# Performance work log

Measured on AMD Instinct MI355X. Metric: run time of the kernel, lower is better.

The kernel has to match this reference:

```python
import jax, jax.numpy as jnp
import numpy as np

D = 1024      # hidden_size
H = 16        # num_attention_heads
HD = D // H   # head_dim
FF = 4096     # intermediate_size
EPS = 1e-5

def layernorm(x, g, b):
    mu = jnp.mean(x, axis=-1, keepdims=True)
    var = jnp.mean(jnp.square(x - mu), axis=-1, keepdims=True)
    return (x - mu) * jax.lax.rsqrt(var + EPS) * g + b

def setup_inputs() -> dict:
    key = jax.random.key(0)
    ks = jax.random.split(key, 16)
    s = 0.02
    return {
        "x":   jax.random.normal(ks[0], (4, 1024, D), jnp.float32),
        "wq":  jax.random.normal(ks[1], (D, D), jnp.float32) * s,
        "bq":  jnp.zeros((D,), jnp.float32),
        "wk":  jax.random.normal(ks[2], (D, D), jnp.float32) * s,
        "bk":  jnp.zeros((D,), jnp.float32),
        "wv":  jax.random.normal(ks[3], (D, D), jnp.float32) * s,
        "bv":  jnp.zeros((D,), jnp.float32),
        "wo":  jax.random.normal(ks[4], (D, D), jnp.float32) * s,
        "bo":  jnp.zeros((D,), jnp.float32),
        "w1":  jax.random.normal(ks[5], (D, FF), jnp.float32) * s,
        "b1":  jnp.zeros((FF,), jnp.float32),
        "w2":  jax.random.normal(ks[6], (FF, D), jnp.float32) * s,
        "b2":  jnp.zeros((D,), jnp.float32),
        "ln1_g": jnp.ones((D,), jnp.float32),
        "ln1_b": jnp.zeros((D,), jnp.float32),
        "ln2_g": jnp.ones((D,), jnp.float32),
        "ln2_b": jnp.zeros((D,), jnp.float32),
    }

def reference(x, wq, bq, wk, bk, wv, bv, wo, bo, w1, b1, w2, b2,
              ln1_g, ln1_b, ln2_g, ln2_b):
    B, S, _ = x.shape
    # --- pre-LN multi-head attention (per-head linears fused as one GEMM) ---
    h = layernorm(x, ln1_g, ln1_b)
    q = (h @ wq + bq).reshape(B, S, H, HD).transpose(0, 2, 1, 3)  # [B,H,S,hd]
    k = (h @ wk + bk).reshape(B, S, H, HD).transpose(0, 2, 1, 3)
    v = (h @ wv + bv).reshape(B, S, H, HD).transpose(0, 2, 1, 3)
    scores = jnp.einsum('bhqd,bhkd->bhqk', q, k) / np.sqrt(HD).astype(x.dtype)
    weights = jax.nn.softmax(scores, axis=-1)  # dropout p=0 -> identity
    attn = jnp.einsum('bhqk,bhkd->bhqd', weights, v)
    attn = attn.transpose(0, 2, 1, 3).reshape(B, S, D)
    x = x + attn @ wo + bo
    # --- pre-LN feed-forward with exact GELU ---
    h2 = layernorm(x, ln2_g, ln2_b)
    ffn = jax.nn.gelu(h2 @ w1 + b1, approximate=False) @ w2 + b2
    return x + ffn
```

## Files before the change

### kernel.cpp

```cpp
#include <hip/hip_runtime.h>
#include <hip/hip_bf16.h>
#include <cstdint>

#define S_LEN  1024
#define DMODEL 1024
#define NTOK   4096
#define NHEAD  16
#define HDIM   64
#define FFDIM  4096
#define NBATCH 4

using bf16x8 = __attribute__((ext_vector_type(8))) short;
using f32x4  = __attribute__((ext_vector_type(4))) float;

__device__ __forceinline__ ushort f2bf(float f) {
  union { float f; uint32_t u; } a; a.f = f;
  uint32_t u = a.u;
  u += 0x7FFFu + ((u >> 16) & 1u);
  return (ushort)(u >> 16);
}
__device__ __forceinline__ float bf2f(ushort u) {
  union { uint32_t u; float f; } c; c.u = ((uint32_t)u) << 16; return c.f;
}
__device__ __forceinline__ float ld_as_float(const float* p, long i) { return p[i]; }
__device__ __forceinline__ float ld_as_float(const ushort* p, long i) { return bf2f(p[i]); }
__device__ __forceinline__ void st_out(float* C, long i, float v) { C[i] = v; }
__device__ __forceinline__ void st_out(ushort* C, long i, float v) { C[i] = f2bf(v); }

__device__ __forceinline__ void gld_lds16(const void* g, void* l) {
  __builtin_amdgcn_global_load_lds((const __attribute__((address_space(1))) void*)g,
                                   (__attribute__((address_space(3))) void*)l, 16, 0, 0);
}

__global__ __launch_bounds__(256) void ln_kernel(const float* __restrict__ x,
    const float* __restrict__ g, const float* __restrict__ b,
    ushort* __restrict__ out) {
  int row = blockIdx.x;
  int tid = threadIdx.x;
  const float4* xr = (const float4*)(x + (long)row * DMODEL);
  float4 v = xr[tid];
  float s  = v.x + v.y + v.z + v.w;
  float s2 = v.x*v.x + v.y*v.y + v.z*v.z + v.w*v.w;
  for (int off = 32; off; off >>= 1) { s += __shfl_down(s, off); s2 += __shfl_down(s2, off); }
  __shared__ float red[8];
  int wid = tid >> 6, lane = tid & 63;
  if (lane == 0) { red[wid] = s; red[wid + 4] = s2; }
  __syncthreads();
  if (tid == 0) {
    red[0] = red[0] + red[1] + red[2] + red[3];
    red[4] = red[4] + red[5] + red[6] + red[7];
  }
  __syncthreads();
  float mu  = red[0] * (1.0f / DMODEL);
  float var = red[4] * (1.0f / DMODEL) - mu * mu;
  float rs  = rsqrtf(var + 1e-5f);
  float4 gg = ((const float4*)g)[tid];
  float4 bb = ((const float4*)b)[tid];
  ushort4 o;
  o.x = f2bf((v.x - mu) * rs * gg.x + bb.x);
  o.y = f2bf((v.y - mu) * rs * gg.y + bb.y);
  o.z = f2bf((v.z - mu) * rs * gg.z + bb.z);
  o.w = f2bf((v.w - mu) * rs * gg.w + bb.w);
  ((ushort4*)(out + (long)row * DMODEL))[tid] = o;
}

__global__ __launch_bounds__(256) void concat3(const float* __restrict__ a,
    const float* __restrict__ b, const float* __restrict__ c, float* __restrict__ o) {
  int i = blockIdx.x * 256 + threadIdx.x;
  o[i] = (i < 1024) ? a[i] : ((i < 2048) ? b[i - 1024] : c[i - 2048]);
}

template <int NP, bool XRES>
__global__ __launch_bounds__(256) void reduce_add(
    const ushort* __restrict__ parts, const float* __restrict__ xres,
    const float* __restrict__ bias, float* __restrict__ out) {
  long i = (long)blockIdx.x * 256 + threadIdx.x;
  const long PSTRIDE = (long)NTOK * DMODEL / 4;
  float4 acc = XRES ? ((const float4*)xres)[i] : ((const float4*)out)[i];
  float4 b = ((const float4*)bias)[i & 255];
  acc.x += b.x; acc.y += b.y; acc.z += b.z; acc.w += b.w;
#pragma unroll
  for (int z = 0; z < NP; ++z) {
    ushort4 u = ((const ushort4*)parts)[z * PSTRIDE + i];
    acc.x += bf2f(u.x); acc.y += bf2f(u.y); acc.z += bf2f(u.z); acc.w += bf2f(u.w);
  }
  ((float4*)out)[i] = acc;
}

template <typename TIN>
__global__ __launch_bounds__(256) void transpose_cvt(const TIN* __restrict__ in,
    ushort* __restrict__ out, int ldin, int ldout,
    long inZhi, long inZlo, long outZ) {
  int z = blockIdx.z;
  in  += (long)(z >> 4) * inZhi + (long)(z & 15) * inZlo;
  out += (long)z * outZ;
  __shared__ float tile[32][33];
  int c0 = blockIdx.x * 32, r0 = blockIdx.y * 32;
  int tx = threadIdx.x, ty = threadIdx.y;
  for (int i = ty; i < 32; i += 8)
    tile[i][tx] = ld_as_float(in, (long)(r0 + i) * ldin + c0 + tx);
  __syncthreads();
  for (int i = ty; i < 32; i += 8)
    out[(long)(c0 + i) * ldout + r0 + tx] = f2bf(tile[tx][i]);
}

template <int ACT, bool BIAS, bool RES, typename TOUT>
__global__ __launch_bounds__(256) void gemm_bt(
    const ushort* __restrict__ A, const ushort* __restrict__ BT, TOUT* __restrict__ C,
    const float* __restrict__ bias, const float* __restrict__ resp,
    int M, int K, int lda, int ldb, int ldc,
    long aZhi, long aZlo, long bZhi, long bZlo, long cZhi, long cZlo) {
  __shared__ __align__(16) ushort lA[2][128 * 64];
  __shared__ __align__(16) ushort lB[2][128 * 64];
  int z = blockIdx.z;
  A  += (long)(z >> 4) * aZhi + (long)(z & 15) * aZlo;
  BT += (long)(z >> 4) * bZhi + (long)(z & 15) * bZlo;
  long coff = (long)(z >> 4) * cZhi + (long)(z & 15) * cZlo;
  int gx = gridDim.x;
  int nwg = gx * gridDim.y;
  int lin = blockIdx.x + gx * blockIdx.y;
  int wg = (lin & 7) * (nwg >> 3) + (lin >> 3);
  int n0 = (wg / gx) * 128, m0 = (wg % gx) * 128;
  int tid = threadIdx.x, lane = tid & 63, wid = tid >> 6;
  int wr = wid >> 1, wc = wid & 1;
  int lrow = lane >> 3;
  int swz = ((lane & 7) ^ lrow) << 3;
  int Mm1 = M - 1;
  f32x4 acc[4][4];
#pragma unroll
  for (int i = 0; i < 4; i++)
#pragma unroll
    for (int j = 0; j < 4; j++) acc[i][j] = (f32x4){0.f, 0.f, 0.f, 0.f};

  auto STAGE = [&](int kt, int buf) {
    const ushort* Ak = A + (kt << 6) + swz;
    const ushort* Bk = BT + (kt << 6) + swz;
#pragma unroll
    for (int c = 0; c < 4; ++c) {
      int ch = (wid << 2) | c;
      int rb = (ch << 3) + lrow;
      gld_lds16(Ak + (long)(n0 + rb) * lda, &lA[buf][ch << 9]);
      int mrow = min(m0 + rb, Mm1);
      gld_lds16(Bk + (long)mrow * ldb, &lB[buf][ch << 9]);
    }
  };

  int nK = K >> 6;
  STAGE(0, 0);
  for (int kt = 0; kt < nK; ++kt) {
    int cur = kt & 1;
    if (kt + 1 < nK) {
      STAGE(kt + 1, cur ^ 1);
      asm volatile("s_waitcnt vmcnt(8)" ::: "memory");
    } else {
      asm volatile("s_waitcnt vmcnt(0)" ::: "memory");
    }
    __builtin_amdgcn_s_barrier();
    __builtin_amdgcn_sched_barrier(0);
#pragma unroll
    for (int kk = 0; kk < 2; ++kk) {
      int g = (kk << 2) | (lane >> 4);
      int kfs = ((g ^ (lane & 7)) << 3);
      bf16x8 af[4], bfr[4];
#pragma unroll
      for (int i = 0; i < 4; i++) {
        af[i]  = *(const bf16x8*)(&lA[cur][((wr << 6) + (i << 4) + (lane & 15)) * 64 + kfs]);
        bfr[i] = *(const bf16x8*)(&lB[cur][((wc << 6) + (i << 4) + (lane & 15)) * 64 + kfs]);
      }
#pragma unroll
      for (int i = 0; i < 4; i++)
#pragma unroll
        for (int j = 0; j < 4; j++)
          acc[i][j] = __builtin_amdgcn_mfma_f32_16x16x32_bf16(af[i], bfr[j], acc[i][j], 0, 0, 0);
    }
    asm volatile("s_waitcnt lgkmcnt(0)" ::: "memory");
    __builtin_amdgcn_s_barrier();
    __builtin_amdgcn_sched_barrier(0);
  }
#pragma unroll
  for (int i = 0; i < 4; i++) {
    int rbase = n0 + wr * 64 + i * 16 + ((lane >> 4) << 2);
#pragma unroll
    for (int j = 0; j < 4; j++) {
      int col = m0 + wc * 64 + j * 16 + (lane & 15);
      if (col < M) {
        float bv = BIAS ? bias[col] : 0.0f;
#pragma unroll
        for (int q = 0; q < 4; q++) {
          int rowg = rbase + q;
          float vv = acc[i][j][q] + bv;
          if (ACT == 1) vv = 0.5f * vv * (1.0f + erff(vv * 0.70710678118f));
          long idx = coff + (long)rowg * ldc + col;
          if (RES) vv += resp[idx];
          st_out(C, idx, vv);
        }
      }
    }
  }
}

template <int ACT, bool BIAS, typename TOUT>
__global__ __launch_bounds__(512, 2) void gemm256(
    const ushort* __restrict__ A, const ushort* __restrict__ BT, TOUT* __restrict__ C,
    const float* __restrict__ bias,
    int K, int lda, int ldb, int ldc, long aZlo, long bZlo, long cZlo) {
  __shared__ __align__(16) ushort lA[2][256 * 64];
  __shared__ __align__(16) ushort lB[2][256 * 64];
  int z = blockIdx.z;
  A  += (long)z * aZlo;
  BT += (long)z * bZlo;
  C  += (long)z * cZlo;
  int gx = gridDim.x;
  int nwg = gx * gridDim.y;
  int lin = blockIdx.x + gx * blockIdx.y;
  int wg = (lin & 7) * (nwg >> 3) + (lin >> 3);
  int n0 = (wg / gx) * 256, m0 = (wg % gx) * 256;
  int tid = threadIdx.x, lane = tid & 63, wid = tid >> 6;
  int wm = wid >> 2, wn = wid & 3;
  int lo = lane & 15, hi = lane >> 4;
  int l7 = lane & 7;
  int srow = tid >> 3;
  int skg  = (tid & 7) ^ (srow & 7);
  const ushort* gA = A + (long)(n0 + srow) * lda + (skg << 3);
  const ushort* gB = BT + (long)(m0 + srow) * ldb + (skg << 3);

  f32x4 acc[8][4];
#pragma unroll
  for (int i = 0; i < 8; ++i)
#pragma unroll
    for (int j = 0; j < 4; ++j) acc[i][j] = (f32x4){0.f, 0.f, 0.f, 0.f};

  auto STG = [&](int kt, int buf, int c) {
    if (c < 4)
      gld_lds16(gA + (long)(c * 64) * lda + (kt << 6), &lA[buf][c * 4096 + wid * 512]);
    else
      gld_lds16(gB + (long)((c - 4) * 64) * ldb + (kt << 6), &lB[buf][(c - 4) * 4096 + wid * 512]);
  };

  int nK = K >> 6;
  STG(0, 0, 4); STG(0, 0, 5); STG(0, 0, 6); STG(0, 0, 7);
  STG(0, 0, 0); STG(0, 0, 1); STG(0, 0, 2); STG(0, 0, 3);
  STG(1, 1, 4); STG(1, 1, 5); STG(1, 1, 6); STG(1, 1, 7);
  asm volatile("s_waitcnt vmcnt(4)" ::: "memory");
  __builtin_amdgcn_s_barrier();

  for (int t = 0; t < nK; ++t) {
    int cur = t & 1, nxt = cur ^ 1;
    ushort* plA = &lA[cur][0];
    ushort* plB = &lB[cur][0];
    bf16x8 bfr[4][2];
#pragma unroll
    for (int p = 0; p < 4; ++p) {
      if (p == 0) {
#pragma unroll
        for (int j = 0; j < 4; ++j)
#pragma unroll
          for (int kk = 0; kk < 2; ++kk)
            bfr[j][kk] = *(const bf16x8*)&plB[(wn * 64 + j * 16 + lo) * 64 +
                                             ((((kk << 2) | hi) ^ l7) << 3)];
      }
      bf16x8 afr[2][2];
#pragma unroll
      for (int ii = 0; ii < 2; ++ii)
#pragma unroll
        for (int kk = 0; kk < 2; ++kk)
          afr[ii][kk] = *(const bf16x8*)&plA[(wm * 128 + (p * 2 + ii) * 16 + lo) * 64 +
                                             ((((kk << 2) | hi) ^ l7) << 3)];
      if (p == 0 && t + 1 < nK) { STG(t + 1, nxt, 0); STG(t + 1, nxt, 1); }
      if (p == 1 && t + 1 < nK) { STG(t + 1, nxt, 2); STG(t + 1, nxt, 3); }
      if (p == 2 && t + 2 < nK) { STG(t + 2, cur, 4); STG(t + 2, cur, 5); }
      if (p == 3 && t + 2 < nK) { STG(t + 2, cur, 6); STG(t + 2, cur, 7); }
      __builtin_amdgcn_s_barrier();
      asm volatile("s_waitcnt lgkmcnt(0)" ::: "memory");
      __builtin_amdgcn_sched_barrier(0);
      __builtin_amdgcn_s_setprio(1);
#pragma unroll
      for (int ii = 0; ii < 2; ++ii)
#pragma unroll
        for (int j = 0; j < 4; ++j)
#pragma unroll
          for (int kk = 0; kk < 2; ++kk)
            acc[p * 2 + ii][j] = __builtin_amdgcn_mfma_f32_16x16x32_bf16(
                afr[ii][kk], bfr[j][kk], acc[p * 2 + ii][j], 0, 0, 0);
      __builtin_amdgcn_s_setprio(0);
      __builtin_amdgcn_sched_barrier(0);
      if (p == 3 && t + 1 < nK) {
        if (t + 2 < nK) asm volatile("s_waitcnt vmcnt(4)" ::: "memory");
        else            asm volatile("s_waitcnt vmcnt(0)" ::: "memory");
      }
      __builtin_amdgcn_s_barrier();
    }
  }

#pragma unroll
  for (int i = 0; i < 8; ++i) {
    int rbase = n0 + wm * 128 + i * 16 + hi * 4;
#pragma unroll
    for (int j = 0; j < 4; ++j) {
      int colg = m0 + wn * 64 + j * 16 + lo;
      float bv = BIAS ? bias[colg] : 0.0f;
#pragma unroll
      for (int q = 0; q < 4; ++q) {
        float vv = acc[i][j][q] + bv;
        if (ACT == 1) vv = 0.5f * vv * (1.0f + erff(vv * 0.70710678118f));
        long idx = (long)(rbase + q) * ldc + colg;
        st_out(C, idx, vv);
      }
    }
  }
}

#define QBLK 64
#define KBLK 128
__global__ __launch_bounds__(256) void flash_attn(
    const ushort* __restrict__ qkv, const ushort* __restrict__ vt,
    ushort* __restrict__ attn) {
  __shared__ __align__(16) ushort lK[2][KBLK * 64];
  __shared__ __align__(16) ushort lV[2][64 * KBLK];
  __shared__ __align__(16) ushort lP[4 * 16 * KBLK];

  int qt = blockIdx.x, bh = blockIdx.z;
  int b = bh >> 4, hh = bh & 15;
  int tid = threadIdx.x, lane = tid & 63, wid = tid >> 6;
  int lo = lane & 15, hi = lane >> 4;
  int lrow = lane >> 3;
  int swz8 = ((lane & 7) ^ lrow) << 3;

  const ushort* Qg = qkv + (long)(b * 1024 + qt * QBLK) * 3072 + hh * 64;
  const ushort* Kg = qkv + (long)(b * 1024) * 3072 + 1024 + hh * 64;
  const ushort* Vg = vt + (long)bh * 64 * 1024;
  ushort* lPw = lP + wid * (16 * KBLK);

  auto STAGE = [&](int t, int buf) {
#pragma unroll
    for (int c = 0; c < 4; ++c) {
      int ch = (wid << 2) | c;
      int rb = (ch << 3) + lrow;
      gld_lds16(Kg + (long)(t * KBLK + rb) * 3072 + swz8, &lK[buf][ch << 9]);
    }
#pragma unroll
    for (int c = 0; c < 4; ++c) {
      int ch = (wid << 2) | c;
      int hd = (ch << 2) + hi;
      gld_lds16(Vg + (long)hd * 1024 + t * KBLK + ((lo ^ (hd & 7)) << 3), &lV[buf][ch << 9]);
    }
  };

#pragma unroll
  for (int c = 0; c < 2; ++c) {
    int ch = wid * 2 + c;
    int rb = ch * 8 + lrow;
    gld_lds16(Qg + (long)rb * 3072 + swz8, &lP[ch << 9]);
  }
  STAGE(0, 0);
  asm volatile("s_waitcnt vmcnt(8)" ::: "memory");
  __builtin_amdgcn_sched_barrier(0);
  bf16x8 a_q[2];
#pragma unroll
  for (int kk = 0; kk < 2; ++kk)
    a_q[kk] = *(const bf16x8*)&lP[(wid * 16 + lo) * 64 + (((kk * 4 + hi) ^ (lo & 7)) << 3)];
  asm volatile("s_waitcnt lgkmcnt(0)" ::: "memory");
  __builtin_amdgcn_sched_barrier(0);
  __builtin_amdgcn_s_barrier();

  float m_run[4], l_run[4];
#pragma unroll
  for (int q = 0; q < 4; ++q) { m_run[q] = -1e30f; l_run[q] = 0.0f; }
  f32x4 acc_o[4];
#pragma unroll
  for (int j = 0; j < 4; ++j) acc_o[j] = (f32x4){0.f, 0.f, 0.f, 0.f};

  for (int t = 0; t < 8; ++t) {
    int cur = t & 1;
    if (t + 1 < 8) {
      STAGE(t + 1, cur ^ 1);
      asm volatile("s_waitcnt vmcnt(8)" ::: "memory");
    } else {
      asm volatile("s_waitcnt vmcnt(0)" ::: "memory");
    }
    __builtin_amdgcn_s_barrier();
    __builtin_amdgcn_sched_barrier(0);

    f32x4 s[8];
#pragma unroll
    for (int j = 0; j < 8; ++j) s[j] = (f32x4){0.f, 0.f, 0.f, 0.f};
#pragma unroll
    for (int kk = 0; kk < 2; ++kk) {
      int slot = ((kk * 4 + hi) ^ (lo & 7)) << 3;
#pragma unroll
      for (int j = 0; j < 8; ++j) {
        bf16x8 bk = *(const bf16x8*)&lK[cur][(j * 16 + lo) * 64 + slot];
        s[j] = __builtin_amdgcn_mfma_f32_16x16x32_bf16(a_q[kk], bk, s[j], 0, 0, 0);
      }
    }
#pragma unroll
    for (int j = 0; j < 8; ++j)
#pragma unroll
      for (int q = 0; q < 4; ++q) s[j][q] *= 0.125f;

    float alpha[4];
#pragma unroll
    for (int q = 0; q < 4; ++q) {
      float m = fmaxf(fmaxf(fmaxf(s[0][q], s[1][q]), fmaxf(s[2][q], s[3][q])),
                      fmaxf(fmaxf(s[4][q], s[5][q]), fmaxf(s[6][q], s[7][q])));
#pragma unroll
      for (int off = 1; off < 16; off <<= 1) m = fmaxf(m, __shfl_xor(m, off));
      float mnew = fmaxf(m_run[q], m);
      alpha[q] = __expf(m_run[q] - mnew);
      m_run[q] = mnew;
    }
    float psum[4] = {0.f, 0.f, 0.f, 0.f};
#pragma unroll
    for (int j = 0; j < 8; ++j)
#pragma unroll
      for (int q = 0; q < 4; ++q) {
        float e = __expf(s[j][q] - m_run[q]);
        psum[q] += e;
        int row = hi * 4 + q;
        int col = j * 16 + lo;
        lPw[row * KBLK + (col ^ ((row & 7) << 3))] = f2bf(e);
      }
#pragma unroll
    for (int q = 0; q < 4; ++q) {
#pragma unroll
      for (int off = 1; off < 16; off <<= 1) psum[q] += __shfl_xor(psum[q], off);
      l_run[q] = l_run[q] * alpha[q] + psum[q];
    }

#pragma unroll
    for (int j = 0; j < 4; ++j)
#pragma unroll
      for (int q = 0; q < 4; ++q) acc_o[j][q] *= alpha[q];
#pragma unroll
    for (int ks = 0; ks < 4; ++ks) {
      int slot = ((ks * 4 + hi) ^ (lo & 7)) << 3;
      bf16x8 ap = *(const bf16x8*)&lPw[lo * KBLK + slot];
#pragma unroll
      for (int j = 0; j < 4; ++j) {
        bf16x8 bv = *(const bf16x8*)&lV[cur][(j * 16 + lo) * KBLK + slot];
        acc_o[j] = __builtin_amdgcn_mfma_f32_16x16x32_bf16(ap, bv, acc_o[j], 0, 0, 0);
      }
    }
    asm volatile("s_waitcnt lgkmcnt(0)" ::: "memory");
    __builtin_amdgcn_s_barrier();
    __builtin_amdgcn_sched_barrier(0);
  }

#pragma unroll
  for (int q = 0; q < 4; ++q) {
    float linv = 1.0f / l_run[q];
    int qrow = qt * QBLK + wid * 16 + hi * 4 + q;
#pragma unroll
    for (int j = 0; j < 4; ++j)
      attn[(long)(b * 1024 + qrow) * 1024 + hh * 64 + j * 16 + lo] = f2bf(acc_o[j][q] * linv);
  }
}

extern "C" void kernel_launch(void* const* d_in, const int* in_sizes, int n_in,
                              void* d_out, int out_size, void* d_ws, size_t ws_size,
                              hipStream_t stream) {
  const float* x    = (const float*)d_in[0];
  const float* wq   = (const float*)d_in[1];
  const float* bq   = (const float*)d_in[2];
  const float* wk   = (const float*)d_in[3];
  const float* bk   = (const float*)d_in[4];
  const float* wv   = (const float*)d_in[5];
  const float* bv   = (const float*)d_in[6];
  const float* wo   = (const float*)d_in[7];
  const float* bo   = (const float*)d_in[8];
  const float* w1   = (const float*)d_in[9];
  const float* b1   = (const float*)d_in[10];
  const float* w2   = (const float*)d_in[11];
  const float* b2   = (const float*)d_in[12];
  const float* ln1g = (const float*)d_in[13];
  const float* ln1b = (const float*)d_in[14];
  const float* ln2g = (const float*)d_in[15];
  const float* ln2b = (const float*)d_in[16];
  float* out = (float*)d_out;

  char* ws = (char*)d_ws;
  size_t off = 0;
  auto alloc = [&](size_t bytes) { void* p = ws + off; off += (bytes + 255) & ~(size_t)255; return p; };
  ushort* h     = (ushort*)alloc((size_t)NTOK * DMODEL * 2);
  ushort* wqkvT = (ushort*)alloc((size_t)3 * DMODEL * DMODEL * 2);
  ushort* woT   = (ushort*)alloc((size_t)DMODEL * DMODEL * 2);
  float*  bqkv  = (float*)alloc((size_t)3 * DMODEL * 4);
  ushort* qkv   = (ushort*)alloc((size_t)NTOK * 3 * DMODEL * 2);
  ushort* vt    = (ushort*)alloc((size_t)64 * HDIM * S_LEN * 2);
  ushort* attn  = (ushort*)alloc((size_t)NTOK * DMODEL * 2);
  ushort* w1T   = (ushort*)alloc((size_t)DMODEL * FFDIM * 2);
  ushort* w2T   = (ushort*)alloc((size_t)FFDIM * DMODEL * 2);
  ushort* gact  = (ushort*)alloc((size_t)NTOK * FFDIM * 2);
  ushort* woPart  = qkv;
  ushort* ffnPart = qkv;

  dim3 tb32(32, 8);
  hipLaunchKernelGGL((transpose_cvt<float>), dim3(DMODEL/32, DMODEL/32, 1), tb32, 0, stream,
                     wq, wqkvT, DMODEL, DMODEL, 0, 0, 0);
  hipLaunchKernelGGL((transpose_cvt<float>), dim3(DMODEL/32, DMODEL/32, 1), tb32, 0, stream,
                     wk, wqkvT + (size_t)DMODEL * DMODEL, DMODEL, DMODEL, 0, 0, 0);
  hipLaunchKernelGGL((transpose_cvt<float>), dim3(DMODEL/32, DMODEL/32, 1), tb32, 0, stream,
                     wv, wqkvT + (size_t)2 * DMODEL * DMODEL, DMODEL, DMODEL, 0, 0, 0);
  hipLaunchKernelGGL((transpose_cvt<float>), dim3(DMODEL/32, DMODEL/32, 1), tb32, 0, stream,
                     wo, woT, DMODEL, DMODEL, 0, 0, 0);
  hipLaunchKernelGGL(concat3, dim3(12), dim3(256), 0, stream, bq, bk, bv, bqkv);

  hipLaunchKernelGGL(ln_kernel, dim3(NTOK), dim3(256), 0, stream, x, ln1g, ln1b, h);

  hipLaunchKernelGGL((gemm256<0, true, ushort>), dim3(12, 16, 1), dim3(512), 0, stream,
                     h, wqkvT, qkv, bqkv, DMODEL, DMODEL, DMODEL, 3 * DMODEL, 0L, 0L, 0L);

  hipLaunchKernelGGL((transpose_cvt<ushort>), dim3(HDIM/32, S_LEN/32, 64), tb32, 0, stream,
                     qkv + 2 * DMODEL, vt, 3 * DMODEL, S_LEN,
                     (long)S_LEN * 3 * DMODEL, 64L, (long)HDIM * S_LEN);

  hipLaunchKernelGGL(flash_attn, dim3(16, 1, 64), dim3(256), 0, stream, qkv, vt, attn);

  hipLaunchKernelGGL((gemm_bt<0, false, false, ushort>), dim3(8, 32, 2), dim3(256), 0, stream,
                     attn, woT, woPart, (const float*)nullptr, (const float*)nullptr,
                     DMODEL, 512, DMODEL, DMODEL, DMODEL,
                     0L, 512L, 0L, 512L, 0L, (long)NTOK * DMODEL);
  hipLaunchKernelGGL((reduce_add<2, true>), dim3(4096), dim3(256), 0, stream,
                     woPart, x, bo, out);
  hipLaunchKernelGGL(ln_kernel, dim3(NTOK), dim3(256), 0, stream, out, ln2g, ln2b, h);
  hipLaunchKernelGGL((transpose_cvt<float>), dim3(FFDIM/32, DMODEL/32, 1), tb32, 0, stream,
                     w1, w1T, FFDIM, DMODEL, 0, 0, 0);
  hipLaunchKernelGGL((transpose_cvt<float>), dim3(DMODEL/32, FFDIM/32, 1), tb32, 0, stream,
                     w2, w2T, DMODEL, FFDIM, 0, 0, 0);
  hipLaunchKernelGGL((gemm256<1, true, ushort>), dim3(16, 16, 1), dim3(512), 0, stream,
                     h, w1T, gact, b1, DMODEL, DMODEL, DMODEL, FFDIM, 0L, 0L, 0L);
  hipLaunchKernelGGL((gemm256<0, false, ushort>), dim3(4, 16, 4), dim3(512), 0, stream,
                     gact, w2T, ffnPart, (const float*)nullptr,
                     1024, FFDIM, FFDIM, DMODEL, 1024L, 1024L, (long)NTOK * DMODEL);
  hipLaunchKernelGGL((reduce_add<4, false>), dim3(4096), dim3(256), 0, stream,
                     ffnPart, (const float*)nullptr, b2, out);
  (void)in_sizes; (void)n_in; (void)out_size; (void)ws_size;
}
```

Measured before the change: 264.8 us.

## Fold softmax scale into Q GEMM, MFMA row sums, fuse residual-reduce with LN2

The QKV GEMM epilogue now multiplies Q columns by log2(e)/sqrt(hd), so flash attention can use exp2 without a per-score scale multiply. The softmax row sum is computed by an extra MFMA against a ones vector instead of shuffle reductions. The kernel also uses a hardware bf16 convert and adds s_setprio hints around the MFMA blocks. Separately, the attention-output reduction and the second layernorm are fused into one kernel, removing one full pass over the activations. In exchange, Q is rounded to bf16 after scaling and the row sum is built from bf16-rounded probabilities.

```diff
diff --git a/kernel.cpp b/kernel.cpp
--- a/kernel.cpp
+++ b/kernel.cpp
@@ -9,6 +9,7 @@
 #define HDIM   64
 #define FFDIM  4096
 #define NBATCH 4
+#define QSCALE 0.1803368801f
 
 using bf16x8 = __attribute__((ext_vector_type(8))) short;
 using f32x4  = __attribute__((ext_vector_type(4))) float;
@@ -18,6 +19,11 @@
   uint32_t u = a.u;
   u += 0x7FFFu + ((u >> 16) & 1u);
   return (ushort)(u >> 16);
+}
+__device__ __forceinline__ ushort f2bf_hw(float f) {
+  uint32_t r;
+  asm("v_cvt_pk_bf16_f32 %0, %1, %1" : "=v"(r) : "v"(f));
+  return (ushort)r;
 }
 __device__ __forceinline__ float bf2f(ushort u) {
   union { uint32_t u; float f; } c; c.u = ((uint32_t)u) << 16; return c.f;
@@ -70,13 +76,13 @@
   o[i] = (i < 1024) ? a[i] : ((i < 2048) ? b[i - 1024] : c[i - 2048]);
 }
 
-template <int NP, bool XRES>
+template <int NP>
 __global__ __launch_bounds__(256) void reduce_add(
-    const ushort* __restrict__ parts, const float* __restrict__ xres,
-    const float* __restrict__ bias, float* __restrict__ out) {
+    const ushort* __restrict__ parts, const float* __restrict__ bias,
+    float* __restrict__ out) {
   long i = (long)blockIdx.x * 256 + threadIdx.x;
   const long PSTRIDE = (long)NTOK * DMODEL / 4;
-  float4 acc = XRES ? ((const float4*)xres)[i] : ((const float4*)out)[i];
+  float4 acc = ((const float4*)out)[i];
   float4 b = ((const float4*)bias)[i & 255];
   acc.x += b.x; acc.y += b.y; acc.z += b.z; acc.w += b.w;
 #pragma unroll
@@ -85,6 +91,49 @@
     acc.x += bf2f(u.x); acc.y += bf2f(u.y); acc.z += bf2f(u.z); acc.w += bf2f(u.w);
   }
   ((float4*)out)[i] = acc;
+}
+
+template <int NP>
+__global__ __launch_bounds__(256) void reduce_ln(
+    const ushort* __restrict__ parts, const float* __restrict__ xres,
+    const float* __restrict__ bias, float* __restrict__ out,
+    const float* __restrict__ g, const float* __restrict__ bln,
+    ushort* __restrict__ hout) {
+  int row = blockIdx.x, tid = threadIdx.x;
+  long i = (long)row * 256 + tid;
+  const long PSTRIDE = (long)NTOK * DMODEL / 4;
+  float4 v = ((const float4*)xres)[i];
+  float4 b = ((const float4*)bias)[tid];
+  v.x += b.x; v.y += b.y; v.z += b.z; v.w += b.w;
+#pragma unroll
+  for (int z = 0; z < NP; ++z) {
+    ushort4 u = ((const ushort4*)parts)[z * PSTRIDE + i];
+    v.x += bf2f(u.x); v.y += bf2f(u.y); v.z += bf2f(u.z); v.w += bf2f(u.w);
+  }
+  ((float4*)out)[i] = v;
+  float s  = v.x + v.y + v.z + v.w;
+  float s2 = v.x*v.x + v.y*v.y + v.z*v.z + v.w*v.w;
+  for (int off = 32; off; off >>= 1) { s += __shfl_down(s, off); s2 += __shfl_down(s2, off); }
+  __shared__ float red[8];
+  int wid = tid >> 6, lane = tid & 63;
+  if (lane == 0) { red[wid] = s; red[wid + 4] = s2; }
+  __syncthreads();
+  if (tid == 0) {
+    red[0] = red[0] + red[1] + red[2] + red[3];
+    red[4] = red[4] + red[5] + red[6] + red[7];
+  }
+  __syncthreads();
+  float mu  = red[0] * (1.0f / DMODEL);
+  float var = red[4] * (1.0f / DMODEL) - mu * mu;
+  float rs  = rsqrtf(var + 1e-5f);
+  float4 gg = ((const float4*)g)[tid];
+  float4 bb = ((const float4*)bln)[tid];
+  ushort4 o;
+  o.x = f2bf((v.x - mu) * rs * gg.x + bb.x);
+  o.y = f2bf((v.y - mu) * rs * gg.y + bb.y);
+  o.z = f2bf((v.z - mu) * rs * gg.z + bb.z);
+  o.w = f2bf((v.w - mu) * rs * gg.w + bb.w);
+  ((ushort4*)hout)[i] = o;
 }
 
 template <typename TIN>
@@ -303,6 +352,7 @@
       for (int q = 0; q < 4; ++q) {
         float vv = acc[i][j][q] + bv;
         if (ACT == 1) vv = 0.5f * vv * (1.0f + erff(vv * 0.70710678118f));
+        if (ACT == 2 && colg < DMODEL) vv *= QSCALE;
         long idx = (long)(rbase + q) * ldc + colg;
         st_out(C, idx, vv);
       }
@@ -331,6 +381,10 @@
   const ushort* Vg = vt + (long)bh * 64 * 1024;
   ushort* lPw = lP + wid * (16 * KBLK);
 
+  bf16x8 kOnes;
+#pragma unroll
+  for (int i = 0; i < 8; ++i) kOnes[i] = (short)0x3F80;
+
   auto STAGE = [&](int t, int buf) {
 #pragma unroll
     for (int c = 0; c < 4; ++c) {
@@ -363,12 +417,13 @@
   __builtin_amdgcn_sched_barrier(0);
   __builtin_amdgcn_s_barrier();
 
-  float m_run[4], l_run[4];
-#pragma unroll
-  for (int q = 0; q < 4; ++q) { m_run[q] = -1e30f; l_run[q] = 0.0f; }
+  float m_run[4];
+#pragma unroll
+  for (int q = 0; q < 4; ++q) m_run[q] = -1e30f;
   f32x4 acc_o[4];
 #pragma unroll
   for (int j = 0; j < 4; ++j) acc_o[j] = (f32x4){0.f, 0.f, 0.f, 0.f};
+  f32x4 acc_l = (f32x4){0.f, 0.f, 0.f, 0.f};
 
   for (int t = 0; t < 8; ++t) {
     int cur = t & 1;
@@ -384,6 +439,7 @@
     f32x4 s[8];
 #pragma unroll
     for (int j = 0; j < 8; ++j) s[j] = (f32x4){0.f, 0.f, 0.f, 0.f};
+    __builtin_amdgcn_s_setprio(1);
 #pragma unroll
     for (int kk = 0; kk < 2; ++kk) {
       int slot = ((kk * 4 + hi) ^ (lo & 7)) << 3;
@@ -393,10 +449,7 @@
         s[j] = __builtin_amdgcn_mfma_f32_16x16x32_bf16(a_q[kk], bk, s[j], 0, 0, 0);
       }
     }
-#pragma unroll
-    for (int j = 0; j < 8; ++j)
-#pragma unroll
-      for (int q = 0; q < 4; ++q) s[j][q] *= 0.125f;
+    __builtin_amdgcn_s_setprio(0);
 
     float alpha[4];
 #pragma unroll
@@ -406,41 +459,38 @@
 #pragma unroll
       for (int off = 1; off < 16; off <<= 1) m = fmaxf(m, __shfl_xor(m, off));
       float mnew = fmaxf(m_run[q], m);
-      alpha[q] = __expf(m_run[q] - mnew);
+      alpha[q] = __builtin_amdgcn_exp2f(m_run[q] - mnew);
       m_run[q] = mnew;
     }
-    float psum[4] = {0.f, 0.f, 0.f, 0.f};
 #pragma unroll
     for (int j = 0; j < 8; ++j)
 #pragma unroll
       for (int q = 0; q < 4; ++q) {
-        float e = __expf(s[j][q] - m_run[q]);
-        psum[q] += e;
+        float e = __builtin_amdgcn_exp2f(s[j][q] - m_run[q]);
         int row = hi * 4 + q;
         int col = j * 16 + lo;
-        lPw[row * KBLK + (col ^ ((row & 7) << 3))] = f2bf(e);
-      }
-#pragma unroll
-    for (int q = 0; q < 4; ++q) {
-#pragma unroll
-      for (int off = 1; off < 16; off <<= 1) psum[q] += __shfl_xor(psum[q], off);
-      l_run[q] = l_run[q] * alpha[q] + psum[q];
-    }
-
+        lPw[row * KBLK + (col ^ ((row & 7) << 3))] = f2bf_hw(e);
+      }
+
+#pragma unroll
+    for (int q = 0; q < 4; ++q) acc_l[q] *= alpha[q];
 #pragma unroll
     for (int j = 0; j < 4; ++j)
 #pragma unroll
       for (int q = 0; q < 4; ++q) acc_o[j][q] *= alpha[q];
+    __builtin_amdgcn_s_setprio(1);
 #pragma unroll
     for (int ks = 0; ks < 4; ++ks) {
       int slot = ((ks * 4 + hi) ^ (lo & 7)) << 3;
       bf16x8 ap = *(const bf16x8*)&lPw[lo * KBLK + slot];
+      acc_l = __builtin_amdgcn_mfma_f32_16x16x32_bf16(ap, kOnes, acc_l, 0, 0, 0);
 #pragma unroll
       for (int j = 0; j < 4; ++j) {
         bf16x8 bv = *(const bf16x8*)&lV[cur][(j * 16 + lo) * KBLK + slot];
         acc_o[j] = __builtin_amdgcn_mfma_f32_16x16x32_bf16(ap, bv, acc_o[j], 0, 0, 0);
       }
     }
+    __builtin_amdgcn_s_setprio(0);
     asm volatile("s_waitcnt lgkmcnt(0)" ::: "memory");
     __builtin_amdgcn_s_barrier();
     __builtin_amdgcn_sched_barrier(0);
@@ -448,7 +498,7 @@
 
 #pragma unroll
   for (int q = 0; q < 4; ++q) {
-    float linv = 1.0f / l_run[q];
+    float linv = 1.0f / acc_l[q];
     int qrow = qt * QBLK + wid * 16 + hi * 4 + q;
 #pragma unroll
     for (int j = 0; j < 4; ++j)
@@ -507,7 +557,7 @@
 
   hipLaunchKernelGGL(ln_kernel, dim3(NTOK), dim3(256), 0, stream, x, ln1g, ln1b, h);
 
-  hipLaunchKernelGGL((gemm256<0, true, ushort>), dim3(12, 16, 1), dim3(512), 0, stream,
+  hipLaunchKernelGGL((gemm256<2, true, ushort>), dim3(12, 16, 1), dim3(512), 0, stream,
                      h, wqkvT, qkv, bqkv, DMODEL, DMODEL, DMODEL, 3 * DMODEL, 0L, 0L, 0L);
 
   hipLaunchKernelGGL((transpose_cvt<ushort>), dim3(HDIM/32, S_LEN/32, 64), tb32, 0, stream,
@@ -520,9 +570,8 @@
                      attn, woT, woPart, (const float*)nullptr, (const float*)nullptr,
                      DMODEL, 512, DMODEL, DMODEL, DMODEL,
                      0L, 512L, 0L, 512L, 0L, (long)NTOK * DMODEL);
-  hipLaunchKernelGGL((reduce_add<2, true>), dim3(4096), dim3(256), 0, stream,
-                     woPart, x, bo, out);
-  hipLaunchKernelGGL(ln_kernel, dim3(NTOK), dim3(256), 0, stream, out, ln2g, ln2b, h);
+  hipLaunchKernelGGL((reduce_ln<2>), dim3(4096), dim3(256), 0, stream,
+                     woPart, x, bo, out, ln2g, ln2b, h);
   hipLaunchKernelGGL((transpose_cvt<float>), dim3(FFDIM/32, DMODEL/32, 1), tb32, 0, stream,
                      w1, w1T, FFDIM, DMODEL, 0, 0, 0);
   hipLaunchKernelGGL((transpose_cvt<float>), dim3(DMODEL/32, FFDIM/32, 1), tb32, 0, stream,
@@ -532,7 +581,7 @@
   hipLaunchKernelGGL((gemm256<0, false, ushort>), dim3(4, 16, 4), dim3(512), 0, stream,
                      gact, w2T, ffnPart, (const float*)nullptr,
                      1024, FFDIM, FFDIM, DMODEL, 1024L, 1024L, (long)NTOK * DMODEL);
-  hipLaunchKernelGGL((reduce_add<4, false>), dim3(4096), dim3(256), 0, stream,
-                     ffnPart, (const float*)nullptr, b2, out);
+  hipLaunchKernelGGL((reduce_add<4>), dim3(4096), dim3(256), 0, stream,
+                     ffnPart, b2, out);
   (void)in_sizes; (void)n_in; (void)out_size; (void)ws_size;
 }
```

New measurement: 252.9 us. 4.5% less time.
